# Kernel optimization log

Measured on AMD Instinct MI355X. Metric: run time of the kernel, lower is better.

Reference implementation:

```python
import jax, jax.numpy as jnp
import numpy as np
from jax import lax

B, T, C_IN = 64, 1000, 12
D_MODEL, D_STATE, D_CONV, EXPAND = 128, 16, 4, 2
D_INNER = EXPAND * D_MODEL          # 256
DT_RANK = (D_MODEL + 15) // 16      # ceil(d_model/16) = 8
NUM_CLASSES = 5


def setup_inputs() -> dict:
    key = jax.random.key(0)
    ks = jax.random.split(key, 12)
    s = 0.05
    f = jnp.float32
    return {
        "x": jax.random.normal(ks[0], (B, T, C_IN), f),
        # input projection Linear(C_IN, D_MODEL) with bias
        "ip_w": jax.random.normal(ks[1], (D_MODEL, C_IN), f) * s,
        "ip_b": jnp.zeros((D_MODEL,), f),
        # Mamba block params (mamba_ssm layout)
        "in_proj_w": jax.random.normal(ks[2], (2 * D_INNER, D_MODEL), f) * s,
        "conv_w": jax.random.normal(ks[3], (D_INNER, D_CONV), f) * s,
        "conv_b": jnp.zeros((D_INNER,), f),
        "x_proj_w": jax.random.normal(ks[4], (DT_RANK + 2 * D_STATE, D_INNER), f) * s,
        "dt_proj_w": jax.random.normal(ks[5], (D_INNER, DT_RANK), f) * s,
        "dt_proj_b": jax.random.uniform(ks[6], (D_INNER,), f, -4.0, -2.0),  # softplus -> small positive dt
        "A_log": jnp.log(jnp.tile(jnp.arange(1, D_STATE + 1, dtype=f), (D_INNER, 1))),
        "D_skip": jnp.ones((D_INNER,), f),
        "out_proj_w": jax.random.normal(ks[7], (D_MODEL, D_INNER), f) * s,
        # classifier head: Linear(128,64) -> ReLU -> Linear(64,5)
        "fc1_w": jax.random.normal(ks[8], (64, D_MODEL), f) * s,
        "fc1_b": jnp.zeros((64,), f),
        "fc2_w": jax.random.normal(ks[9], (NUM_CLASSES, 64), f) * s,
        "fc2_b": jnp.zeros((NUM_CLASSES,), f),
    }


def _silu(x):
    return x * jax.nn.sigmoid(x)


def _mamba(h, in_proj_w, conv_w, conv_b, x_proj_w, dt_proj_w, dt_proj_b,
           A_log, D_skip, out_proj_w):
    # h: (B, T, D_MODEL)
    xz = h @ in_proj_w.T                              # (B, T, 2*Di)
    xm, z = jnp.split(xz, 2, axis=-1)
    # depthwise causal conv over time (pad left d_conv-1)
    xp = jnp.pad(xm, ((0, 0), (D_CONV - 1, 0), (0, 0)))
    rhs = conv_w.T[:, None, :]                        # (d_conv, 1, Di)
    xc = lax.conv_general_dilated(
        xp, rhs, (1,), 'VALID',
        dimension_numbers=('NHC', 'HIO', 'NHC'),
        feature_group_count=D_INNER) + conv_b
    u = _silu(xc)                                     # (B, T, Di)
    dbc = u @ x_proj_w.T                              # (B, T, dt_rank + 2N)
    dt = dbc[..., :DT_RANK]
    Bm = dbc[..., DT_RANK:DT_RANK + D_STATE]          # (B, T, N)
    Cm = dbc[..., DT_RANK + D_STATE:]                 # (B, T, N)
    delta = jax.nn.softplus(dt @ dt_proj_w.T + dt_proj_b)  # (B, T, Di)
    A = -jnp.exp(A_log)                               # (Di, N)

    def step(hst, inp):
        d_t, b_t, c_t, u_t = inp                      # (B,Di),(B,N),(B,N),(B,Di)
        dA = jnp.exp(d_t[..., None] * A)              # (B, Di, N)
        hst = dA * hst + (d_t * u_t)[..., None] * b_t[:, None, :]
        y_t = jnp.einsum('bdn,bn->bd', hst, c_t)
        return hst, y_t

    h0 = jnp.zeros((h.shape[0], D_INNER, D_STATE), h.dtype)
    _, ys = lax.scan(step, h0, (delta.transpose(1, 0, 2), Bm.transpose(1, 0, 2),
                                Cm.transpose(1, 0, 2), u.transpose(1, 0, 2)))
    y = ys.transpose(1, 0, 2) + u * D_skip            # (B, T, Di)
    y = y * _silu(z)
    return y @ out_proj_w.T                           # (B, T, D_MODEL)


def reference(x, ip_w, ip_b, in_proj_w, conv_w, conv_b, x_proj_w, dt_proj_w,
              dt_proj_b, A_log, D_skip, out_proj_w, fc1_w, fc1_b, fc2_w, fc2_b):
    h = x @ ip_w.T + ip_b                             # (B, T, D_MODEL)
    y = _mamba(h, in_proj_w, conv_w, conv_b, x_proj_w, dt_proj_w, dt_proj_b,
               A_log, D_skip, out_proj_w)
    last = y[:, -1, :]                                # (B, D_MODEL)
    hid = jax.nn.relu(last @ fc1_w.T + fc1_b)
    return hid @ fc2_w.T + fc2_b                      # (B, NUM_CLASSES)
```

## Files before the change

### kernel.cpp

```cpp
#include <hip/hip_runtime.h>
#include <cstddef>

#define T_LEN 1000
#define B_SZ 64
#define C_IN_ 12
#define D_MODEL_ 128
#define D_INNER_ 256
#define D_STATE_ 16
#define DT_RANK_ 8
#define N_CLS 5
#define NCH 10
#define CIT 25

typedef __attribute__((ext_vector_type(8))) short bf16x8;
typedef __attribute__((ext_vector_type(8))) unsigned short u16x8;
typedef __attribute__((ext_vector_type(4))) float f32x4;

__device__ __forceinline__ float fast_exp2(float x) {
#if __has_builtin(__builtin_amdgcn_exp2f)
  return __builtin_amdgcn_exp2f(x);
#else
  float r; asm volatile("v_exp_f32 %0, %1" : "=v"(r) : "v"(x)); return r;
#endif
}
__device__ __forceinline__ float fast_log2(float x) {
#if __has_builtin(__builtin_amdgcn_logf)
  return __builtin_amdgcn_logf(x);
#else
  float r; asm volatile("v_log_f32 %0, %1" : "=v"(r) : "v"(x)); return r;
#endif
}
__device__ __forceinline__ float fast_rcp(float x) {
#if __has_builtin(__builtin_amdgcn_rcpf)
  return __builtin_amdgcn_rcpf(x);
#else
  float r; asm volatile("v_rcp_f32 %0, %1" : "=v"(r) : "v"(x)); return r;
#endif
}
__device__ __forceinline__ float silu_f(float x) {
  float den = 1.f + fast_exp2(-x * 1.4426950408889634f);
  return x * fast_rcp(den);
}
__device__ __forceinline__ float softplus_f(float x) {
  const float L = 1.4426950408889634f, iL = 0.6931471805599453f;
  float e = fast_exp2(-fabsf(x) * L);
  float l = fast_log2(1.f + e) * iL;
  return fmaxf(x, 0.f) + l;
}
__device__ __forceinline__ unsigned short f2bf(float f) {
  unsigned u = __builtin_bit_cast(unsigned, f);
  u = u + 0x7FFFu + ((u >> 16) & 1u);
  return (unsigned short)(u >> 16);
}
__device__ __forceinline__ float bf2f(unsigned short h) {
  unsigned u = ((unsigned)h) << 16;
  return __builtin_bit_cast(float, u);
}

__global__ __launch_bounds__(256) void k0_prep(
    const float* __restrict__ x, const float* __restrict__ ip_w,
    const float* __restrict__ ip_b, const float* __restrict__ in_proj_w,
    char* __restrict__ h_pk, char* __restrict__ w_pk)
{
  __shared__ unsigned short pk_s[8192];
  __shared__ unsigned short pkw_s[32768];
  const int tid = threadIdx.x;

  if (blockIdx.x == 16) {
    if (blockIdx.y != 0) return;
    const int n = tid;
    for (int k = 0; k < D_MODEL_; ++k) {
      unsigned short v = f2bf(in_proj_w[(size_t)n * D_MODEL_ + k]);
      int off = ((n >> 4) * 4 + (k >> 5)) * 512 + ((k & 31) >> 3) * 128
              + (n & 15) * 8 + (k & 7);
      pkw_s[off] = v;
    }
    __syncthreads();
    const float4* s4 = (const float4*)pkw_s;
    float4* dst = (float4*)w_pk;
#pragma unroll
    for (int q = 0; q < 16; ++q) dst[tid * 16 + q] = s4[tid * 16 + q];
    return;
  }

  const int tile4 = blockIdx.x;
  const int b = blockIdx.y;
  const int rl = tid & 63;
  const int kc = (tid >> 6) * 32;
  const int t = tile4 * 64 + rl;

  float xr[C_IN_] = {0.f, 0.f, 0.f, 0.f, 0.f, 0.f, 0.f, 0.f, 0.f, 0.f, 0.f, 0.f};
  const bool valid = (t < T_LEN);
  if (valid) {
    const float4* xp = (const float4*)(x + ((size_t)b * T_LEN + t) * C_IN_);
    float4 v0 = xp[0], v1 = xp[1], v2 = xp[2];
    xr[0] = v0.x; xr[1] = v0.y; xr[2] = v0.z;  xr[3] = v0.w;
    xr[4] = v1.x; xr[5] = v1.y; xr[6] = v1.z;  xr[7] = v1.w;
    xr[8] = v2.x; xr[9] = v2.y; xr[10] = v2.z; xr[11] = v2.w;
  }
  for (int kk = 0; kk < 32; ++kk) {
    const int k = kc + kk;
    unsigned short v = 0;
    if (valid) {
      float acc = ip_b[k];
      const float* wr = ip_w + k * C_IN_;
#pragma unroll
      for (int c = 0; c < C_IN_; ++c) acc += xr[c] * wr[c];
      v = f2bf(acc);
    }
    int off = (rl >> 4) * 2048 + (k >> 5) * 512 + ((k & 31) >> 3) * 128
            + (rl & 15) * 8 + (k & 7);
    pk_s[off] = v;
  }
  __syncthreads();
  const float4* s4 = (const float4*)pk_s;
  float4* dst = (float4*)(h_pk + (size_t)(b * 64 + tile4 * 4) * 4096);
#pragma unroll
  for (int q = 0; q < 4; ++q) dst[tid * 4 + q] = s4[tid * 4 + q];
}

__global__ __launch_bounds__(256) void k1_u(
    const char* __restrict__ h_pk, const char* __restrict__ w_pk,
    const float* __restrict__ conv_w, const float* __restrict__ conv_b,
    float* __restrict__ u_out)
{
  __shared__ float xm[67][260];

  const int tile = blockIdx.x;
  const int b    = blockIdx.y;
  const int t0   = tile * 64;
  const int tid  = threadIdx.x;
  const int w    = tid >> 6;
  const int l    = tid & 63;

  {
    const char* achunk = h_pk + (size_t)(b * 64 + tile * 4 + w) * 4096;
    bf16x8 a0 = *(const bf16x8*)(achunk + 0 * 1024 + l * 16);
    bf16x8 a1 = *(const bf16x8*)(achunk + 1 * 1024 + l * 16);
    bf16x8 a2 = *(const bf16x8*)(achunk + 2 * 1024 + l * 16);
    bf16x8 a3 = *(const bf16x8*)(achunk + 3 * 1024 + l * 16);

    const int row_l = w * 16 + (l >> 4) * 4;
#pragma unroll
    for (int nt = 0; nt < 16; ++nt) {
      const char* wb = w_pk + (size_t)nt * 4096 + l * 16;
      bf16x8 b0 = *(const bf16x8*)(wb + 0 * 1024);
      bf16x8 b1 = *(const bf16x8*)(wb + 1 * 1024);
      bf16x8 b2 = *(const bf16x8*)(wb + 2 * 1024);
      bf16x8 b3 = *(const bf16x8*)(wb + 3 * 1024);
      f32x4 acc = {0.f, 0.f, 0.f, 0.f};
      acc = __builtin_amdgcn_mfma_f32_16x16x32_bf16(a0, b0, acc, 0, 0, 0);
      acc = __builtin_amdgcn_mfma_f32_16x16x32_bf16(a1, b1, acc, 0, 0, 0);
      acc = __builtin_amdgcn_mfma_f32_16x16x32_bf16(a2, b2, acc, 0, 0, 0);
      acc = __builtin_amdgcn_mfma_f32_16x16x32_bf16(a3, b3, acc, 0, 0, 0);
      const int col = nt * 16 + (l & 15);
#pragma unroll
      for (int r = 0; r < 4; ++r)
        xm[3 + row_l + r][col] = acc[r];
    }
  }

  if (tile > 0) {
    const char* hchunk = h_pk + (size_t)(b * 64 + tile * 4 - 1) * 4096;
    bf16x8 ha0 = *(const bf16x8*)(hchunk + 0 * 1024 + l * 16);
    bf16x8 ha1 = *(const bf16x8*)(hchunk + 1 * 1024 + l * 16);
    bf16x8 ha2 = *(const bf16x8*)(hchunk + 2 * 1024 + l * 16);
    bf16x8 ha3 = *(const bf16x8*)(hchunk + 3 * 1024 + l * 16);
#pragma unroll
    for (int q = 0; q < 4; ++q) {
      const int nt = w * 4 + q;
      const char* wb = w_pk + (size_t)nt * 4096 + l * 16;
      bf16x8 b0 = *(const bf16x8*)(wb + 0 * 1024);
      bf16x8 b1 = *(const bf16x8*)(wb + 1 * 1024);
      bf16x8 b2 = *(const bf16x8*)(wb + 2 * 1024);
      bf16x8 b3 = *(const bf16x8*)(wb + 3 * 1024);
      f32x4 acc = {0.f, 0.f, 0.f, 0.f};
      acc = __builtin_amdgcn_mfma_f32_16x16x32_bf16(ha0, b0, acc, 0, 0, 0);
      acc = __builtin_amdgcn_mfma_f32_16x16x32_bf16(ha1, b1, acc, 0, 0, 0);
      acc = __builtin_amdgcn_mfma_f32_16x16x32_bf16(ha2, b2, acc, 0, 0, 0);
      acc = __builtin_amdgcn_mfma_f32_16x16x32_bf16(ha3, b3, acc, 0, 0, 0);
      if (l >= 48) {
        const int col = nt * 16 + (l & 15);
        xm[0][col] = acc[1];
        xm[1][col] = acc[2];
        xm[2][col] = acc[3];
      }
    }
  } else {
#pragma unroll
    for (int r = 0; r < 3; ++r) xm[r][tid] = 0.f;
  }
  __syncthreads();

  {
    const int n = tid;
    const float4 cw = *(const float4*)&conv_w[n * 4];
    const float  cb = conv_b[n];
    float x0 = xm[0][n], x1 = xm[1][n], x2 = xm[2][n];
    for (int i = 0; i < 64; ++i) {
      const int t = t0 + i;
      float x3 = xm[3 + i][n];
      if (t < T_LEN) {
        float s = cb + x0 * cw.x + x1 * cw.y + x2 * cw.z + x3 * cw.w;
        u_out[(((size_t)b * T_LEN + t) << 8) + n] = silu_f(s);
      }
      x0 = x1; x1 = x2; x2 = x3;
    }
  }
}

__global__ __launch_bounds__(256) void k3_delta(
    const float* __restrict__ u, const float* __restrict__ x_proj_w,
    const float* __restrict__ dt_proj_w, const float* __restrict__ dt_proj_b,
    float* __restrict__ delta_T, float* __restrict__ du_T,
    float* __restrict__ bm_plain, float* __restrict__ u_last)
{
  __shared__ __align__(16) float smem[24 * 65 * 4];
  float4 (*xp4)[65] = reinterpret_cast<float4(*)[65]>(smem);
  float* tx = smem;
  __shared__ float dt_s[64][9];
  __shared__ float bm_s[64][17];

  const int row0 = blockIdx.x * 64;
  const int tid = threadIdx.x;

  for (int f = tid; f < 24 * 64; f += 256) {
    int c = f >> 6, k4 = f & 63;
    xp4[c][k4] = *(const float4*)&x_proj_w[(size_t)c * 256 + k4 * 4];
  }
  const float4 w0 = *(const float4*)&dt_proj_w[(size_t)tid * 8];
  const float4 w1 = *(const float4*)&dt_proj_w[(size_t)tid * 8 + 4];
  const float bias = dt_proj_b[tid];
  __syncthreads();

  {
    const int r2 = tid >> 3, cg = tid & 7;
    const int ra = 2 * r2;
    const float4* ua4 = (const float4*)(u + (size_t)(row0 + ra) * 256);
    const float4* ub4 = (const float4*)(u + (size_t)(row0 + ra + 1) * 256);
    float a0 = 0.f, a1 = 0.f, a2 = 0.f, b0 = 0.f, b1 = 0.f, b2 = 0.f;
    for (int k4 = 0; k4 < 64; ++k4) {
      float4 a = ua4[k4], bb = ub4[k4];
      float4 q0 = xp4[cg * 3 + 0][k4];
      float4 q1 = xp4[cg * 3 + 1][k4];
      float4 q2 = xp4[cg * 3 + 2][k4];
      a0 += a.x * q0.x + a.y * q0.y + a.z * q0.z + a.w * q0.w;
      a1 += a.x * q1.x + a.y * q1.y + a.z * q1.z + a.w * q1.w;
      a2 += a.x * q2.x + a.y * q2.y + a.z * q2.z + a.w * q2.w;
      b0 += bb.x * q0.x + bb.y * q0.y + bb.z * q0.z + bb.w * q0.w;
      b1 += bb.x * q1.x + bb.y * q1.y + bb.z * q1.z + bb.w * q1.w;
      b2 += bb.x * q2.x + bb.y * q2.y + bb.z * q2.z + bb.w * q2.w;
    }
    float va[2][3] = {{a0, a1, a2}, {b0, b1, b2}};
#pragma unroll
    for (int rr = 0; rr < 2; ++rr)
#pragma unroll
      for (int c = 0; c < 3; ++c) {
        int col = cg * 3 + c;
        int row = ra + rr;
        if (col < 8) dt_s[row][col] = va[rr][c];
        else bm_s[row][col - 8] = va[rr][c];
      }
  }
  __syncthreads();

  for (int c16 = 0; c16 < 4; ++c16) {
    float dd[16], uu[16];
#pragma unroll
    for (int j = 0; j < 16; ++j) {
      int r = c16 * 16 + j;
      float pre = bias
        + dt_s[r][0] * w0.x + dt_s[r][1] * w0.y + dt_s[r][2] * w0.z + dt_s[r][3] * w0.w
        + dt_s[r][4] * w1.x + dt_s[r][5] * w1.y + dt_s[r][6] * w1.z + dt_s[r][7] * w1.w;
      float dlt = softplus_f(pre);
      size_t o = (size_t)(row0 + r) * 256 + tid;
      float uv = u[o];
      dd[j] = dlt;
      uu[j] = dlt * uv;
      int rowg = row0 + r;
      if ((rowg - (rowg / 1000) * 1000) == 999)
        u_last[(rowg / 1000) * 256 + tid] = uv;
    }
#pragma unroll
    for (int j = 0; j < 16; ++j) tx[tid * 17 + j] = dd[j];
    __syncthreads();
#pragma unroll
    for (int q = 0; q < 4; ++q) {
      int d_ = (tid >> 2) + 64 * q;
      int t4 = (tid & 3) * 4;
      float4 v = make_float4(tx[d_ * 17 + t4], tx[d_ * 17 + t4 + 1],
                             tx[d_ * 17 + t4 + 2], tx[d_ * 17 + t4 + 3]);
      int rowg = row0 + c16 * 16 + t4;
      int bb = rowg / 1000;
      int t = rowg - bb * 1000;
      *(float4*)&delta_T[((size_t)(bb * 256 + d_)) * 1000 + t] = v;
    }
    __syncthreads();
#pragma unroll
    for (int j = 0; j < 16; ++j) tx[tid * 17 + j] = uu[j];
    __syncthreads();
#pragma unroll
    for (int q = 0; q < 4; ++q) {
      int d_ = (tid >> 2) + 64 * q;
      int t4 = (tid & 3) * 4;
      float4 v = make_float4(tx[d_ * 17 + t4], tx[d_ * 17 + t4 + 1],
                             tx[d_ * 17 + t4 + 2], tx[d_ * 17 + t4 + 3]);
      int rowg = row0 + c16 * 16 + t4;
      int bb = rowg / 1000;
      int t = rowg - bb * 1000;
      *(float4*)&du_T[((size_t)(bb * 256 + d_)) * 1000 + t] = v;
    }
    __syncthreads();
  }
  {
    int idx = tid * 4;
    int row = idx >> 4, n0 = idx & 15;
    float4 v = make_float4(bm_s[row][n0], bm_s[row][n0 + 1],
                           bm_s[row][n0 + 2], bm_s[row][n0 + 3]);
    *(float4*)&bm_plain[((size_t)(row0 + row)) * 16 + n0] = v;
  }
}

__global__ __launch_bounds__(256) void k4_scan(
    const float* __restrict__ delta_T, const float* __restrict__ du_T,
    const float* __restrict__ bm_plain, const float* __restrict__ A_log,
    float* __restrict__ Qb, float* __restrict__ Pb)
{
  __shared__ float da[16][100];
  __shared__ float ua[16][100];
  __shared__ float bs[100][16];

  const int d0 = blockIdx.x * 16;
  const int b  = blockIdx.y;
  const int c  = blockIdx.z;
  const int tid = threadIdx.x;
  const int dl = tid >> 4;
  const int n  = tid & 15;

  for (int f = tid; f < 400; f += 256) {
    int row = f / 25, col = f - row * 25;
    const size_t g = ((size_t)(b * 256 + d0 + row)) * 1000 + c * 100 + col * 4;
    *(float4*)&da[row][col * 4] = *(const float4*)&delta_T[g];
    *(float4*)&ua[row][col * 4] = *(const float4*)&du_T[g];
  }
  for (int f = tid; f < 400; f += 256) {
    ((float4*)bs)[f] = ((const float4*)(bm_plain + ((size_t)b * 1000 + c * 100) * 16))[f];
  }
  const float A2 = -expf(A_log[(size_t)d0 * 16 + tid]) * 1.4426950408889634f;
  __syncthreads();

  float s = 0.f, sum = 0.f;
#pragma unroll
  for (int i = 0; i < CIT; ++i) {
    float4 dv = *(const float4*)&da[dl][4 * i];
    float4 xv = *(const float4*)&ua[dl][4 * i];
    sum += (dv.x + dv.y) + (dv.z + dv.w);
    s = fast_exp2(dv.x * A2) * s + xv.x * bs[4 * i + 0][n];
    s = fast_exp2(dv.y * A2) * s + xv.y * bs[4 * i + 1][n];
    s = fast_exp2(dv.z * A2) * s + xv.z * bs[4 * i + 2][n];
    s = fast_exp2(dv.w * A2) * s + xv.w * bs[4 * i + 3][n];
  }

  const size_t o = (size_t)c * 262144 + (size_t)b * 4096 + (size_t)d0 * 16 + tid;
  Qb[o] = s;
  Pb[o] = fast_exp2(A2 * sum);
}

__global__ __launch_bounds__(256) void k4b_combine(
    const float* __restrict__ Qb, const float* __restrict__ Pb,
    float* __restrict__ state_out)
{
  const size_t g = (size_t)blockIdx.x * 256 + threadIdx.x;
  float s = Qb[g];
#pragma unroll
  for (int c = 1; c < NCH; ++c)
    s = Qb[(size_t)c * 262144 + g] + Pb[(size_t)c * 262144 + g] * s;
  state_out[g] = s;
}

__global__ __launch_bounds__(256) void k5_head(
    const float* __restrict__ x, const float* __restrict__ ip_w,
    const float* __restrict__ ip_b, const float* __restrict__ in_proj_w,
    const float* __restrict__ x_proj_w, const float* __restrict__ u_last,
    const float* __restrict__ state, const float* __restrict__ D_skip,
    const float* __restrict__ out_proj_w, const float* __restrict__ fc1_w,
    const float* __restrict__ fc1_b, const float* __restrict__ fc2_w,
    const float* __restrict__ fc2_b, float* __restrict__ out)
{
  const int b = blockIdx.x, tid = threadIdx.x;
  __shared__ float hl[128], ul[256], zs[256], cm[16], yv[256], ov[128], hid[64];
  if (tid < 128) {
    float acc = ip_b[tid];
    const float* xr = x + ((size_t)b * T_LEN + (T_LEN - 1)) * C_IN_;
#pragma unroll
    for (int c = 0; c < C_IN_; ++c) acc += xr[c] * ip_w[tid * C_IN_ + c];
    hl[tid] = acc;
  }
  ul[tid] = u_last[b * 256 + tid];
  __syncthreads();
  {
    float acc = 0.f;
    const float4* wv = (const float4*)(in_proj_w + (size_t)(256 + tid) * 128);
    const float4* h4 = (const float4*)hl;
    for (int k = 0; k < 32; ++k) {
      float4 a = wv[k], c = h4[k];
      acc += c.x * a.x + c.y * a.y + c.z * a.z + c.w * a.w;
    }
    zs[tid] = silu_f(acc);
  }
  if (tid < 16) {
    float acc = 0.f;
    const float4* wv = (const float4*)(x_proj_w + (size_t)(24 + tid) * 256);
    const float4* u4 = (const float4*)ul;
    for (int k = 0; k < 64; ++k) {
      float4 a = wv[k], c = u4[k];
      acc += c.x * a.x + c.y * a.y + c.z * a.z + c.w * a.w;
    }
    cm[tid] = acc;
  }
  __syncthreads();
  {
    const float* st = state + ((size_t)b * 256 + tid) * 16;
    float acc = 0.f;
#pragma unroll
    for (int n = 0; n < 16; ++n) acc += st[n] * cm[n];
    yv[tid] = (acc + ul[tid] * D_skip[tid]) * zs[tid];
  }
  __syncthreads();
  if (tid < 128) {
    float acc = 0.f;
    const float4* wv = (const float4*)(out_proj_w + (size_t)tid * 256);
    const float4* y4 = (const float4*)yv;
    for (int k = 0; k < 64; ++k) {
      float4 a = wv[k], c = y4[k];
      acc += c.x * a.x + c.y * a.y + c.z * a.z + c.w * a.w;
    }
    ov[tid] = acc;
  }
  __syncthreads();
  if (tid < 64) {
    float acc = fc1_b[tid];
    const float4* wv = (const float4*)(fc1_w + (size_t)tid * 128);
    const float4* o4 = (const float4*)ov;
    for (int k = 0; k < 32; ++k) {
      float4 a = wv[k], c = o4[k];
      acc += c.x * a.x + c.y * a.y + c.z * a.z + c.w * a.w;
    }
    hid[tid] = fmaxf(acc, 0.f);
  }
  __syncthreads();
  if (tid < N_CLS) {
    float acc = fc2_b[tid];
    const float* wv = fc2_w + (size_t)tid * 64;
    for (int k = 0; k < 64; ++k) acc += hid[k] * wv[k];
    out[b * N_CLS + tid] = acc;
  }
}

extern "C" void kernel_launch(void* const* d_in, const int* in_sizes, int n_in,
                              void* d_out, int out_size, void* d_ws, size_t ws_size,
                              hipStream_t stream) {
  (void)in_sizes; (void)n_in; (void)out_size; (void)ws_size;
  const float* x         = (const float*)d_in[0];
  const float* ip_w      = (const float*)d_in[1];
  const float* ip_b      = (const float*)d_in[2];
  const float* in_proj_w = (const float*)d_in[3];
  const float* conv_w    = (const float*)d_in[4];
  const float* conv_b    = (const float*)d_in[5];
  const float* x_proj_w  = (const float*)d_in[6];
  const float* dt_proj_w = (const float*)d_in[7];
  const float* dt_proj_b = (const float*)d_in[8];
  const float* A_log     = (const float*)d_in[9];
  const float* D_skip    = (const float*)d_in[10];
  const float* out_proj_w= (const float*)d_in[11];
  const float* fc1_w     = (const float*)d_in[12];
  const float* fc1_b     = (const float*)d_in[13];
  const float* fc2_w     = (const float*)d_in[14];
  const float* fc2_b     = (const float*)d_in[15];
  float* out = (float*)d_out;

  float* u       = (float*)d_ws;
  float* delta_T = u + (size_t)16384000;
  float* du_T    = delta_T + (size_t)16384000;
  float* bm      = du_T + (size_t)16384000;
  float* state   = bm + (size_t)1024000;
  float* u_last  = state + (size_t)262144;
  char* h_pk = (char*)delta_T;
  char* w_pk = h_pk + (size_t)64 * 64 * 4096;
  float* Qb  = u;
  float* Pb  = u + (size_t)4000000;

  k0_prep<<<dim3(17, 64), 256, 0, stream>>>(x, ip_w, ip_b, in_proj_w, h_pk, w_pk);
  k1_u<<<dim3(16, 64), 256, 0, stream>>>(h_pk, w_pk, conv_w, conv_b, u);
  k3_delta<<<1000, 256, 0, stream>>>(u, x_proj_w, dt_proj_w, dt_proj_b,
                                     delta_T, du_T, bm, u_last);
  k4_scan<<<dim3(16, 64, NCH), 256, 0, stream>>>(delta_T, du_T, bm, A_log, Qb, Pb);
  k4b_combine<<<1024, 256, 0, stream>>>(Qb, Pb, state);
  k5_head<<<64, 256, 0, stream>>>(x, ip_w, ip_b, in_proj_w, x_proj_w, u_last, state,
                                  D_skip, out_proj_w, fc1_w, fc1_b, fc2_w, fc2_b, out);
}
```

Before: 204.7 us.

## Transpose B matrix to time-major and stream scan inputs through registers

k3 now writes the B projection transposed as (batch, state, time), so each scan thread reads a contiguous time run for its own state index. k4_scan no longer stages delta, du and B in shared memory behind a barrier; each thread reads float4 values straight from global memory with a 4-deep register prefetch ring. This removes the LDS staging, the syncthreads and the shared-memory reads. In exchange, threads in a wave that share a channel re-read the same delta/du addresses from global or cache, and B is read with a scattered stride.

```diff
diff --git a/kernel.cpp b/kernel.cpp
--- a/kernel.cpp
+++ b/kernel.cpp
@@ -213,7 +213,7 @@
     const float* __restrict__ u, const float* __restrict__ x_proj_w,
     const float* __restrict__ dt_proj_w, const float* __restrict__ dt_proj_b,
     float* __restrict__ delta_T, float* __restrict__ du_T,
-    float* __restrict__ bm_plain, float* __restrict__ u_last)
+    float* __restrict__ bm_T, float* __restrict__ u_last)
 {
   __shared__ __align__(16) float smem[24 * 65 * 4];
   float4 (*xp4)[65] = reinterpret_cast<float4(*)[65]>(smem);
@@ -313,52 +313,56 @@
     __syncthreads();
   }
   {
-    int idx = tid * 4;
-    int row = idx >> 4, n0 = idx & 15;
-    float4 v = make_float4(bm_s[row][n0], bm_s[row][n0 + 1],
-                           bm_s[row][n0 + 2], bm_s[row][n0 + 3]);
-    *(float4*)&bm_plain[((size_t)(row0 + row)) * 16 + n0] = v;
+    const int n = tid >> 4;
+    const int tq = tid & 15;
+    float4 v = make_float4(bm_s[tq * 4 + 0][n], bm_s[tq * 4 + 1][n],
+                           bm_s[tq * 4 + 2][n], bm_s[tq * 4 + 3][n]);
+    int rowg = row0 + tq * 4;
+    int bb = rowg / 1000;
+    int t = rowg - bb * 1000;
+    *(float4*)&bm_T[((size_t)(bb * 16 + n)) * 1000 + t] = v;
   }
 }
 
 __global__ __launch_bounds__(256) void k4_scan(
     const float* __restrict__ delta_T, const float* __restrict__ du_T,
-    const float* __restrict__ bm_plain, const float* __restrict__ A_log,
+    const float* __restrict__ bm_T, const float* __restrict__ A_log,
     float* __restrict__ Qb, float* __restrict__ Pb)
 {
-  __shared__ float da[16][100];
-  __shared__ float ua[16][100];
-  __shared__ float bs[100][16];
-
   const int d0 = blockIdx.x * 16;
   const int b  = blockIdx.y;
   const int c  = blockIdx.z;
   const int tid = threadIdx.x;
   const int dl = tid >> 4;
   const int n  = tid & 15;
-
-  for (int f = tid; f < 400; f += 256) {
-    int row = f / 25, col = f - row * 25;
-    const size_t g = ((size_t)(b * 256 + d0 + row)) * 1000 + c * 100 + col * 4;
-    *(float4*)&da[row][col * 4] = *(const float4*)&delta_T[g];
-    *(float4*)&ua[row][col * 4] = *(const float4*)&du_T[g];
-  }
-  for (int f = tid; f < 400; f += 256) {
-    ((float4*)bs)[f] = ((const float4*)(bm_plain + ((size_t)b * 1000 + c * 100) * 16))[f];
-  }
-  const float A2 = -expf(A_log[(size_t)d0 * 16 + tid]) * 1.4426950408889634f;
-  __syncthreads();
-
+  const int d  = d0 + dl;
+
+  const float A2 = -expf(A_log[(size_t)d * 16 + n]) * 1.4426950408889634f;
+  const float* dp = delta_T + ((size_t)(b * 256 + d)) * 1000 + c * 100;
+  const float* xp = du_T    + ((size_t)(b * 256 + d)) * 1000 + c * 100;
+  const float* bp = bm_T    + ((size_t)(b * 16 + n)) * 1000 + c * 100;
+
+  float4 db[4], xb[4], bb[4];
+#pragma unroll
+  for (int j = 0; j < 4; ++j) {
+    db[j] = *(const float4*)(dp + 4 * j);
+    xb[j] = *(const float4*)(xp + 4 * j);
+    bb[j] = *(const float4*)(bp + 4 * j);
+  }
   float s = 0.f, sum = 0.f;
 #pragma unroll
   for (int i = 0; i < CIT; ++i) {
-    float4 dv = *(const float4*)&da[dl][4 * i];
-    float4 xv = *(const float4*)&ua[dl][4 * i];
+    float4 dv = db[i & 3], xv = xb[i & 3], bv = bb[i & 3];
+    if (i + 4 < CIT) {
+      db[i & 3] = *(const float4*)(dp + 4 * (i + 4));
+      xb[i & 3] = *(const float4*)(xp + 4 * (i + 4));
+      bb[i & 3] = *(const float4*)(bp + 4 * (i + 4));
+    }
     sum += (dv.x + dv.y) + (dv.z + dv.w);
-    s = fast_exp2(dv.x * A2) * s + xv.x * bs[4 * i + 0][n];
-    s = fast_exp2(dv.y * A2) * s + xv.y * bs[4 * i + 1][n];
-    s = fast_exp2(dv.z * A2) * s + xv.z * bs[4 * i + 2][n];
-    s = fast_exp2(dv.w * A2) * s + xv.w * bs[4 * i + 3][n];
+    s = fast_exp2(dv.x * A2) * s + xv.x * bv.x;
+    s = fast_exp2(dv.y * A2) * s + xv.y * bv.y;
+    s = fast_exp2(dv.z * A2) * s + xv.z * bv.z;
+    s = fast_exp2(dv.w * A2) * s + xv.w * bv.w;
   }
 
   const size_t o = (size_t)c * 262144 + (size_t)b * 4096 + (size_t)d0 * 16 + tid;
```

Measured after the change: 274.2 us. 34.0% more time.
